# Optimization experiments

Hardware: AMD Instinct MI355X
Metric: run time of the kernel (lower is better)

## Reference

```python
import jax, jax.numpy as jnp
import numpy as np

B, T, H, L = 64, 2048, 256, 16


def setup_inputs() -> dict:
    key = jax.random.key(0)
    ks = jax.random.split(key, 6)
    x = jax.random.normal(ks[0], (B, T, H), dtype=jnp.float32)
    tags = jax.random.randint(ks[1], (B, T), 0, L).astype(jnp.int32)
    mask = jnp.ones((B, T), dtype=bool)  # torchcrf requires mask[:,0] all on
    W = jax.random.normal(ks[2], (L, H), dtype=jnp.float32) * (1.0 / np.sqrt(H))
    b = jnp.zeros((L,), dtype=jnp.float32)
    # torchcrf initializes transitions ~ U(-0.1, 0.1)
    start_transitions = jax.random.uniform(ks[3], (L,), minval=-0.1, maxval=0.1)
    end_transitions = jax.random.uniform(ks[4], (L,), minval=-0.1, maxval=0.1)
    transitions = jax.random.uniform(ks[5], (L, L), minval=-0.1, maxval=0.1)
    return {"x": x, "W": W, "b": b,
            "start_transitions": start_transitions,
            "end_transitions": end_transitions,
            "transitions": transitions,
            "tags": tags, "mask": mask}


def reference(x, W, b, start_transitions, end_transitions, transitions, tags, mask):
    # Emitter: Linear(hidden_dim -> num_labels)
    emissions = jnp.einsum('bth,lh->btl', x, W) + b  # [B,T,L]
    maskf = mask.astype(emissions.dtype)             # [B,T]

    # ---- numerator: score of the gold tag path (vectorized, no scan) ----
    emit_gold = jnp.take_along_axis(emissions, tags[..., None].astype(jnp.int32), axis=2)[..., 0]  # [B,T]
    first_tags = tags[:, 0]
    score = start_transitions[first_tags] + emit_gold[:, 0]
    trans_gold = transitions[tags[:, :-1], tags[:, 1:]]  # [B,T-1]
    score = score + jnp.sum((trans_gold + emit_gold[:, 1:]) * maskf[:, 1:], axis=1)
    seq_ends = jnp.sum(mask.astype(jnp.int32), axis=1) - 1  # index of last valid step
    last_tags = jnp.take_along_axis(tags, seq_ends[:, None], axis=1)[:, 0]
    score = score + end_transitions[last_tags]

    # ---- denominator: forward algorithm (log partition) via lax.scan over time ----
    em_t = jnp.swapaxes(emissions, 0, 1)  # [T,B,L]
    mask_t = jnp.swapaxes(mask, 0, 1)     # [T,B]
    alpha0 = start_transitions[None, :] + em_t[0]  # [B,L]

    def step(alpha, inp):
        em, m = inp  # em: [B,L], m: [B]
        # logsumexp over previous label: alpha[b,i] + transitions[i,j] + em[b,j]
        nxt = jax.nn.logsumexp(alpha[:, :, None] + transitions[None, :, :] + em[:, None, :], axis=1)
        alpha = jnp.where(m[:, None], nxt, alpha)
        return alpha, None

    alphaT, _ = jax.lax.scan(step, alpha0, (em_t[1:], mask_t[1:]))
    denom = jax.nn.logsumexp(alphaT + end_transitions[None, :], axis=1)  # [B]

    llh = score - denom          # log-likelihood per sequence
    return -jnp.mean(llh)        # reduction='mean', nll = -crf(...)
```

## Files before the change

kernel.cpp:

```cpp
#include <hip/hip_runtime.h>
#include <math.h>


#define Bb 64
#define Tt 2048
#define Hh 256
#define Ll 16
#define CHUNK 32
#define NC (Tt / CHUNK)
#define ROWS 128
#define TSTR 20

typedef __attribute__((ext_vector_type(8))) short short8;
typedef __attribute__((ext_vector_type(4))) float f32x4;

__device__ __forceinline__ unsigned pk2bf(float a, float b) {
  unsigned ua = __float_as_uint(a) + 0x8000u;
  unsigned ub = __float_as_uint(b) + 0x8000u;
  return (ua >> 16) | (ub & 0xFFFF0000u);
}
__device__ __forceinline__ short8 pack8(float4 lo, float4 hi) {
  union { int4 i; short8 s; } u;
  u.i.x = pk2bf(lo.x, lo.y);
  u.i.y = pk2bf(lo.z, lo.w);
  u.i.z = pk2bf(hi.x, hi.y);
  u.i.w = pk2bf(hi.z, hi.w);
  return u.s;
}

__global__ __launch_bounds__(256) void k_fused(const float* __restrict__ x,
                                               const float* __restrict__ W,
                                               const float* __restrict__ bias,
                                               const float* __restrict__ strans,
                                               const float* __restrict__ etrans,
                                               const float* __restrict__ trans,
                                               const int* __restrict__ tags,
                                               float* __restrict__ em0,
                                               float* __restrict__ Pout,
                                               float* __restrict__ lscale,
                                               float* __restrict__ score) {
  __shared__ float tile[ROWS * TSTR];
  __shared__ unsigned short ghb[ROWS * 16];
  __shared__ float Pbuf[4][16 * TSTR];

  const int tid = threadIdx.x, w = tid >> 6, lane = tid & 63;
  const int n = lane & 15, quad = lane >> 4;
  const int b = blockIdx.x >> 4, blk = blockIdx.x & 15;
  const int gc = blk * 4 + w;

  {
    const float4* wp4 = (const float4*)(W + (size_t)n * Hh) + quad * 2;
    short8 Bf[8];
#pragma unroll
    for (int ks = 0; ks < 8; ++ks) Bf[ks] = pack8(wp4[ks * 8], wp4[ks * 8 + 1]);
    float bs = bias[n];
    size_t Grow = (size_t)blockIdx.x * ROWS + w * 32 + n;
    const float4* xa = (const float4*)(x + Grow * Hh) + quad * 2;
    const float4* xb = (const float4*)(x + (Grow + 16) * Hh) + quad * 2;
    f32x4 acc0 = {0.f, 0.f, 0.f, 0.f}, acc1 = {0.f, 0.f, 0.f, 0.f};
#pragma unroll
    for (int ks = 0; ks < 8; ++ks) {
      short8 a0 = pack8(xa[ks * 8], xa[ks * 8 + 1]);
      short8 a1 = pack8(xb[ks * 8], xb[ks * 8 + 1]);
      acc0 = __builtin_amdgcn_mfma_f32_16x16x32_bf16(a0, Bf[ks], acc0, 0, 0, 0);
      acc1 = __builtin_amdgcn_mfma_f32_16x16x32_bf16(a1, Bf[ks], acc1, 0, 0, 0);
    }
#pragma unroll
    for (int r = 0; r < 4; ++r) {
      tile[(w * 32 + quad * 4 + r) * TSTR + n] = acc0[r] + bs;
      tile[(w * 32 + 16 + quad * 4 + r) * TSTR + n] = acc1[r] + bs;
    }
    if (blk == 0 && w == 0 && quad == 0) em0[b * 16 + n] = acc0[0] + bs;
  }
  __syncthreads();

  {
    float s2 = 0.f;
    if (lane < 32) {
      int rl = w * 32 + lane;
      int t = blk * ROWS + rl;
      int gt = b * Tt + t;
      int tag = tags[gt];
      float ev = tile[rl * TSTR + tag];
      if (t == 0) s2 = strans[tag] + ev;
      else        s2 = trans[tags[gt - 1] * 16 + tag] + ev;
      if (t == Tt - 1) s2 += etrans[tag];
    }
#pragma unroll
    for (int msk = 1; msk < 64; msk <<= 1) s2 += __shfl_xor(s2, msk);
    if (lane == 0) atomicAdd(score + b, s2);
  }

  float offsum = 0.f;
  {
    if (lane < 32) {
      int rl = w * 32 + lane;
      const float4* tp = (const float4*)(tile + rl * TSTR);
      float4 a0 = tp[0], a1 = tp[1], a2 = tp[2], a3 = tp[3];
      float m = fmaxf(fmaxf(fmaxf(fmaxf(a0.x, a0.y), fmaxf(a0.z, a0.w)),
                            fmaxf(fmaxf(a1.x, a1.y), fmaxf(a1.z, a1.w))),
                      fmaxf(fmaxf(fmaxf(a2.x, a2.y), fmaxf(a2.z, a2.w)),
                            fmaxf(fmaxf(a3.x, a3.y), fmaxf(a3.z, a3.w))));
      float4 e0 = make_float4(expf(a0.x - m), expf(a0.y - m), expf(a0.z - m), expf(a0.w - m));
      float4 e1 = make_float4(expf(a1.x - m), expf(a1.y - m), expf(a1.z - m), expf(a1.w - m));
      float4 e2 = make_float4(expf(a2.x - m), expf(a2.y - m), expf(a2.z - m), expf(a2.w - m));
      float4 e3 = make_float4(expf(a3.x - m), expf(a3.y - m), expf(a3.z - m), expf(a3.w - m));
      int4 lo, hi;
      lo.x = pk2bf(e0.x, e0.y); lo.y = pk2bf(e0.z, e0.w);
      lo.z = pk2bf(e1.x, e1.y); lo.w = pk2bf(e1.z, e1.w);
      hi.x = pk2bf(e2.x, e2.y); hi.y = pk2bf(e2.z, e2.w);
      hi.z = pk2bf(e3.x, e3.y); hi.w = pk2bf(e3.z, e3.w);
      ((int4*)ghb)[rl * 2] = lo;
      ((int4*)ghb)[rl * 2 + 1] = hi;
      int t = blk * ROWS + rl;
      offsum = (t >= 1) ? m : 0.f;
    }
#pragma unroll
    for (int msk = 1; msk < 64; msk <<= 1) offsum += __shfl_xor(offsum, msk);
  }
  __syncthreads();

  {
    short8 Eb = {0, 0, 0, 0, 0, 0, 0, 0};
    if (quad < 2) {
      float e[8];
#pragma unroll
      for (int j = 0; j < 8; ++j) e[j] = expf(trans[(quad * 8 + j) * 16 + n]);
      Eb = pack8(make_float4(e[0], e[1], e[2], e[3]), make_float4(e[4], e[5], e[6], e[7]));
    }
    short8 Aid = {0, 0, 0, 0, 0, 0, 0, 0};
    if (quad < 2 && (n >> 3) == quad) ((short*)&Aid)[n & 7] = (short)0x3F80;

    float* Pw = Pbuf[w];
    float off = offsum;
    const int sbeg = (gc == 0) ? 1 : 0;
    const unsigned short* grow = ghb + (w * 32) * 16 + n;
    short8 A = Aid;
    for (int s = sbeg; s < CHUNK; ++s) {
      f32x4 z = {0.f, 0.f, 0.f, 0.f};
      f32x4 d = __builtin_amdgcn_mfma_f32_16x16x32_bf16(A, Eb, z, 0, 0, 0);
      float g = __uint_as_float(((unsigned)grow[s * 16]) << 16);
      d[0] *= g; d[1] *= g; d[2] *= g; d[3] *= g;
      if (((s & 7) == 7) || (s == CHUNK - 1)) {
        float mx = fmaxf(fmaxf(d[0], d[1]), fmaxf(d[2], d[3]));
#pragma unroll
        for (int msk = 1; msk < 64; msk <<= 1) mx = fmaxf(mx, __shfl_xor(mx, msk));
        float inv = __builtin_amdgcn_rcpf(mx);
        d[0] *= inv; d[1] *= inv; d[2] *= inv; d[3] *= inv;
        off += logf(mx);
      }
#pragma unroll
      for (int r = 0; r < 4; ++r) Pw[(quad * 4 + r) * TSTR + n] = d[r];
      if (quad < 2) {
        const float4* pr = (const float4*)(Pw + n * TSTR + quad * 8);
        A = pack8(pr[0], pr[1]);
      }
    }
    {
      int i = lane >> 2, jg = lane & 3;
      float4 pv = *(const float4*)(Pw + i * TSTR + jg * 4);
      ((float4*)(Pout + ((size_t)(b * NC + gc)) * 256))[lane] = pv;
      if (lane == 0) lscale[b * NC + gc] = off;
    }
  }
}

__global__ __launch_bounds__(256) void k_combine(const float* __restrict__ em0,
                                                 const float* __restrict__ P,
                                                 const float* __restrict__ lscale,
                                                 const float* __restrict__ strans,
                                                 const float* __restrict__ etrans,
                                                 float* __restrict__ denom) {
  int b = blockIdx.x, tid = threadIdx.x;
  __shared__ float Pl[NC * 256];
  const float4* src = (const float4*)(P + (size_t)b * NC * 256);
  float4* dst = (float4*)Pl;
  for (int idx = tid; idx < NC * 64; idx += 256) dst[idx] = src[idx];
  __syncthreads();
  if (tid >= 64) return;
  int lane = tid;
  float ls = lscale[b * NC + lane];
#pragma unroll
  for (int m = 1; m < 64; m <<= 1) ls += __shfl_xor(ls, m);

  int j = lane & 15, ig = lane >> 4;
  float a = strans[j] + em0[b * 16 + j];
  float m0 = a;
#pragma unroll
  for (int m = 1; m < 16; m <<= 1) m0 = fmaxf(m0, __shfl_xor(m0, m));
  float v = expf(a - m0);
  float o = m0 + ls;

  for (int cc = 0; cc < NC; ++cc) {
    const float* Pc = Pl + cc * 256;
    float part = 0.f;
#pragma unroll
    for (int r = 0; r < 4; ++r) {
      int srcl = (ig << 4) + ig * 4 + r;
      float vr = __shfl(v, srcl);
      part = fmaf(vr, Pc[(ig * 4 + r) * 16 + j], part);
    }
    part += __shfl_xor(part, 16);
    part += __shfl_xor(part, 32);
    if ((cc & 3) == 3) {
      float mx = part;
#pragma unroll
      for (int m = 1; m < 16; m <<= 1) mx = fmaxf(mx, __shfl_xor(mx, m));
      o += logf(mx);
      v = part * __builtin_amdgcn_rcpf(mx);
    } else {
      v = part;
    }
  }
  float sj = v * expf(etrans[j]);
#pragma unroll
  for (int m = 1; m < 16; m <<= 1) sj += __shfl_xor(sj, m);
  if (lane == 0) denom[b] = o + logf(sj);
}

__global__ __launch_bounds__(64) void k_final(const float* __restrict__ score,
                                              const float* __restrict__ denom,
                                              float* __restrict__ out) {
  int lane = threadIdx.x;
  float llh = score[lane] - denom[lane];
#pragma unroll
  for (int m = 1; m < 64; m <<= 1) llh += __shfl_xor(llh, m);
  if (lane == 0) out[0] = -llh * (1.0f / 64.0f);
}

extern "C" void kernel_launch(void* const* d_in, const int* in_sizes, int n_in,
                              void* d_out, int out_size, void* d_ws, size_t ws_size,
                              hipStream_t stream) {
  const float* x = (const float*)d_in[0];
  const float* W = (const float*)d_in[1];
  const float* bias = (const float*)d_in[2];
  const float* strans = (const float*)d_in[3];
  const float* etrans = (const float*)d_in[4];
  const float* trans = (const float*)d_in[5];
  const int* tags = (const int*)d_in[6];

  float* ws = (float*)d_ws;
  float* em0 = ws;
  float* P = em0 + Bb * 16;
  float* lscale = P + (size_t)Bb * NC * 256;
  float* score = lscale + Bb * NC;
  float* denom = score + Bb;
  float* out = (float*)d_out;

  hipMemsetAsync(score, 0, Bb * sizeof(float), stream);
  hipLaunchKernelGGL(k_fused, dim3(Bb * Tt / ROWS), dim3(256), 0, stream,
                     x, W, bias, strans, etrans, trans, tags, em0, P, lscale, score);
  hipLaunchKernelGGL(k_combine, dim3(Bb), dim3(256), 0, stream, em0, P, lscale, strans, etrans, denom);
  hipLaunchKernelGGL(k_final, dim3(1), dim3(64), 0, stream, score, denom, out);
}
```

Measured before the change: 248.5 us.

## Keep chunk transfer-matrix product in MFMA registers, drop LDS round-trip and renorm

The per-chunk product of transition matrices now uses a 16x16x16 bf16 MFMA laid out so the output accumulator packs directly into the next step's B operand. This removes the per-step LDS store, reload and repack. Periodic max renormalisation is replaced by a constant 0.25 prescale on exp(trans), compensated by a fixed log(4) term per step in the offset. The projection GEMM also preloads x and W into registers in batches, and launch bounds request 4 blocks per SM. The trade-off is a risk of bf16 under- or overflow across 32 unnormalised steps, plus higher register pressure from the preloaded arrays.

```diff
diff --git a/kernel.cpp b/kernel.cpp
--- a/kernel.cpp
+++ b/kernel.cpp
@@ -12,6 +12,7 @@
 #define TSTR 20
 
 typedef __attribute__((ext_vector_type(8))) short short8;
+typedef __attribute__((ext_vector_type(4))) short short4v;
 typedef __attribute__((ext_vector_type(4))) float f32x4;
 
 __device__ __forceinline__ unsigned pk2bf(float a, float b) {
@@ -28,17 +29,28 @@
   return u.s;
 }
 
-__global__ __launch_bounds__(256) void k_fused(const float* __restrict__ x,
-                                               const float* __restrict__ W,
-                                               const float* __restrict__ bias,
-                                               const float* __restrict__ strans,
-                                               const float* __restrict__ etrans,
-                                               const float* __restrict__ trans,
-                                               const int* __restrict__ tags,
-                                               float* __restrict__ em0,
-                                               float* __restrict__ Pout,
-                                               float* __restrict__ lscale,
-                                               float* __restrict__ score) {
+#if __has_builtin(__builtin_amdgcn_mfma_f32_16x16x16bf16_1k)
+#define MFMA16(a, b, c) __builtin_amdgcn_mfma_f32_16x16x16bf16_1k(a, b, c, 0, 0, 0)
+#else
+__device__ __forceinline__ f32x4 mfma16_asm(short4v a, short4v b, f32x4 c) {
+  f32x4 d;
+  asm("v_mfma_f32_16x16x16_bf16 %0, %1, %2, %3" : "=v"(d) : "v"(a), "v"(b), "v"(c));
+  return d;
+}
+#define MFMA16(a, b, c) mfma16_asm(a, b, c)
+#endif
+
+__global__ __launch_bounds__(256, 4) void k_fused(const float* __restrict__ x,
+                                                  const float* __restrict__ W,
+                                                  const float* __restrict__ bias,
+                                                  const float* __restrict__ strans,
+                                                  const float* __restrict__ etrans,
+                                                  const float* __restrict__ trans,
+                                                  const int* __restrict__ tags,
+                                                  float* __restrict__ em0,
+                                                  float* __restrict__ Pout,
+                                                  float* __restrict__ lscale,
+                                                  float* __restrict__ score) {
   __shared__ float tile[ROWS * TSTR];
   __shared__ unsigned short ghb[ROWS * 16];
   __shared__ float Pbuf[4][16 * TSTR];
@@ -50,19 +62,30 @@
 
   {
     const float4* wp4 = (const float4*)(W + (size_t)n * Hh) + quad * 2;
+    float4 wr[16];
+#pragma unroll
+    for (int ks = 0; ks < 8; ++ks) { wr[2 * ks] = wp4[ks * 8]; wr[2 * ks + 1] = wp4[ks * 8 + 1]; }
     short8 Bf[8];
 #pragma unroll
-    for (int ks = 0; ks < 8; ++ks) Bf[ks] = pack8(wp4[ks * 8], wp4[ks * 8 + 1]);
+    for (int ks = 0; ks < 8; ++ks) Bf[ks] = pack8(wr[2 * ks], wr[2 * ks + 1]);
     float bs = bias[n];
     size_t Grow = (size_t)blockIdx.x * ROWS + w * 32 + n;
     const float4* xa = (const float4*)(x + Grow * Hh) + quad * 2;
     const float4* xb = (const float4*)(x + (Grow + 16) * Hh) + quad * 2;
     f32x4 acc0 = {0.f, 0.f, 0.f, 0.f}, acc1 = {0.f, 0.f, 0.f, 0.f};
+    float4 ra[16];
+#pragma unroll
+    for (int ks = 0; ks < 8; ++ks) { ra[2 * ks] = xa[ks * 8]; ra[2 * ks + 1] = xa[ks * 8 + 1]; }
 #pragma unroll
     for (int ks = 0; ks < 8; ++ks) {
-      short8 a0 = pack8(xa[ks * 8], xa[ks * 8 + 1]);
-      short8 a1 = pack8(xb[ks * 8], xb[ks * 8 + 1]);
+      short8 a0 = pack8(ra[2 * ks], ra[2 * ks + 1]);
       acc0 = __builtin_amdgcn_mfma_f32_16x16x32_bf16(a0, Bf[ks], acc0, 0, 0, 0);
+    }
+#pragma unroll
+    for (int ks = 0; ks < 8; ++ks) { ra[2 * ks] = xb[ks * 8]; ra[2 * ks + 1] = xb[ks * 8 + 1]; }
+#pragma unroll
+    for (int ks = 0; ks < 8; ++ks) {
+      short8 a1 = pack8(ra[2 * ks], ra[2 * ks + 1]);
       acc1 = __builtin_amdgcn_mfma_f32_16x16x32_bf16(a1, Bf[ks], acc1, 0, 0, 0);
     }
 #pragma unroll
@@ -121,41 +144,50 @@
   __syncthreads();
 
   {
-    short8 Eb = {0, 0, 0, 0, 0, 0, 0, 0};
-    if (quad < 2) {
-      float e[8];
-#pragma unroll
-      for (int j = 0; j < 8; ++j) e[j] = expf(trans[(quad * 8 + j) * 16 + n]);
-      Eb = pack8(make_float4(e[0], e[1], e[2], e[3]), make_float4(e[4], e[5], e[6], e[7]));
-    }
-    short8 Aid = {0, 0, 0, 0, 0, 0, 0, 0};
-    if (quad < 2 && (n >> 3) == quad) ((short*)&Aid)[n & 7] = (short)0x3F80;
+    union { unsigned u[2]; short4v s4; } ae;
+    {
+      float e0 = 0.25f * expf(trans[(quad * 4 + 0) * 16 + n]);
+      float e1 = 0.25f * expf(trans[(quad * 4 + 1) * 16 + n]);
+      float e2 = 0.25f * expf(trans[(quad * 4 + 2) * 16 + n]);
+      float e3 = 0.25f * expf(trans[(quad * 4 + 3) * 16 + n]);
+      ae.u[0] = pk2bf(e0, e1);
+      ae.u[1] = pk2bf(e2, e3);
+    }
+    union { unsigned u[2]; short sh[4]; short4v s4; } bq;
+    bq.u[0] = 0; bq.u[1] = 0;
+    if ((n >> 2) == quad) bq.sh[n & 3] = (short)0x3F80;
+
+    const int sbeg = (gc == 0) ? 1 : 0;
+    const unsigned short* grow = ghb + (w * 32) * 16 + quad * 4;
+    short4v Bq = bq.s4;
+    f32x4 d;
+#define PSTEP(ss) { \
+      const unsigned* gp = (const unsigned*)(grow + (ss) * 16); \
+      unsigned glo = gp[0], ghi = gp[1]; \
+      f32x4 z = {0.f, 0.f, 0.f, 0.f}; \
+      d = MFMA16(ae.s4, Bq, z); \
+      d[0] *= __uint_as_float(glo << 16); \
+      d[1] *= __uint_as_float(glo & 0xFFFF0000u); \
+      d[2] *= __uint_as_float(ghi << 16); \
+      d[3] *= __uint_as_float(ghi & 0xFFFF0000u); \
+      union { unsigned pu[2]; short4v ps; } pb; \
+      pb.pu[0] = pk2bf(d[0], d[1]); \
+      pb.pu[1] = pk2bf(d[2], d[3]); \
+      Bq = pb.ps; }
+    if (sbeg == 0) PSTEP(0)
+#pragma unroll
+    for (int s = 1; s < CHUNK; ++s) PSTEP(s)
+#undef PSTEP
+
+    float mx = fmaxf(fmaxf(d[0], d[1]), fmaxf(d[2], d[3]));
+#pragma unroll
+    for (int msk = 1; msk < 64; msk <<= 1) mx = fmaxf(mx, __shfl_xor(mx, msk));
+    float inv = __builtin_amdgcn_rcpf(mx);
+    float off = offsum + (float)(CHUNK - sbeg) * 1.3862943611198906f + logf(mx);
 
     float* Pw = Pbuf[w];
-    float off = offsum;
-    const int sbeg = (gc == 0) ? 1 : 0;
-    const unsigned short* grow = ghb + (w * 32) * 16 + n;
-    short8 A = Aid;
-    for (int s = sbeg; s < CHUNK; ++s) {
-      f32x4 z = {0.f, 0.f, 0.f, 0.f};
-      f32x4 d = __builtin_amdgcn_mfma_f32_16x16x32_bf16(A, Eb, z, 0, 0, 0);
-      float g = __uint_as_float(((unsigned)grow[s * 16]) << 16);
-      d[0] *= g; d[1] *= g; d[2] *= g; d[3] *= g;
-      if (((s & 7) == 7) || (s == CHUNK - 1)) {
-        float mx = fmaxf(fmaxf(d[0], d[1]), fmaxf(d[2], d[3]));
-#pragma unroll
-        for (int msk = 1; msk < 64; msk <<= 1) mx = fmaxf(mx, __shfl_xor(mx, msk));
-        float inv = __builtin_amdgcn_rcpf(mx);
-        d[0] *= inv; d[1] *= inv; d[2] *= inv; d[3] *= inv;
-        off += logf(mx);
-      }
-#pragma unroll
-      for (int r = 0; r < 4; ++r) Pw[(quad * 4 + r) * TSTR + n] = d[r];
-      if (quad < 2) {
-        const float4* pr = (const float4*)(Pw + n * TSTR + quad * 8);
-        A = pack8(pr[0], pr[1]);
-      }
-    }
+#pragma unroll
+    for (int r = 0; r < 4; ++r) Pw[n * TSTR + quad * 4 + r] = d[r] * inv;
     {
       int i = lane >> 2, jg = lane & 3;
       float4 pv = *(const float4*)(Pw + i * TSTR + jg * 4);
```

Measured after the change: 241.2 us. -2.9%, faster.
